# Kernel optimization log

Measured on AMD Instinct MI355X. Metric: run time of the kernel, lower is better.

The kernel has to match this reference:

```python
import jax, jax.numpy as jnp
import numpy as np

N_NODES = 100000
N_EDGES = 1250000
IN_FEATS = 64
OUT_FEATS = 64


def setup_inputs() -> dict:
    key = jax.random.key(0)
    k_h, k_src, k_dst, k_w, k_b = jax.random.split(key, 5)
    h = jax.random.normal(k_h, (N_NODES, IN_FEATS), dtype=jnp.float32)
    src = jax.random.randint(k_src, (N_EDGES,), 0, N_NODES, dtype=jnp.int64)
    dst = jax.random.randint(k_dst, (N_EDGES,), 0, N_NODES, dtype=jnp.int64)
    # torch nn.Linear: weight [out, in], bias [out], uniform(-stdv, stdv)
    stdv = 1.0 / np.sqrt(IN_FEATS)
    W = jax.random.uniform(k_w, (OUT_FEATS, IN_FEATS), dtype=jnp.float32, minval=-stdv, maxval=stdv)
    b = jax.random.uniform(k_b, (OUT_FEATS,), dtype=jnp.float32, minval=-stdv, maxval=stdv)
    return {"h": h, "src": src, "dst": dst, "W": W, "b": b}


def reference(h, src, dst, W, b):
    # update_all(copy_src, sum): ah[v] = sum over edges (u->v) of h[u]
    msgs = h[src]                                   # [E, in] irregular gather
    ah = jax.ops.segment_sum(msgs, dst, num_segments=N_NODES)  # [N, in] scatter-add
    out = ah @ W.T + b                              # linear
    return jax.nn.relu(out)
```

## Files before the change

kernel.cpp:

```cpp
#include <hip/hip_runtime.h>

#define N_NODES 100000
#define N_EDGES 1250000
#define FEATS 64

#define NPB   128
#define NBUCK ((N_NODES + NPB - 1) / NPB)
#define CAP   2304
#define TILE  4096
#define NTILES ((N_EDGES + TILE - 1) / TILE)

typedef unsigned short ushort8 __attribute__((ext_vector_type(8)));

__device__ __forceinline__ float bf2f(unsigned short u) {
    return __uint_as_float(((unsigned int)u) << 16);
}
__device__ __forceinline__ unsigned short f2bf(float f) {
    unsigned int x = __float_as_uint(f);
    unsigned int lsb = (x >> 16) & 1u;
    x += 0x7fffu + lsb;
    return (unsigned short)(x >> 16);
}


__global__ __launch_bounds__(256) void binA_pack_kernel(
        const float* __restrict__ h,
        unsigned short* __restrict__ hb,
        const int* __restrict__ src,
        const int* __restrict__ dst,
        int* __restrict__ cursor,
        int* __restrict__ pairs) {
    const int PTOT = N_NODES * FEATS;
    for (int i = (blockIdx.x * 256 + threadIdx.x) * 8; i < PTOT;
         i += gridDim.x * 256 * 8) {
        float4 a = *(const float4*)(h + i);
        float4 c = *(const float4*)(h + i + 4);
        ushort8 u;
        u[0] = f2bf(a.x); u[1] = f2bf(a.y); u[2] = f2bf(a.z); u[3] = f2bf(a.w);
        u[4] = f2bf(c.x); u[5] = f2bf(c.y); u[6] = f2bf(c.z); u[7] = f2bf(c.w);
        *(ushort8*)(hb + i) = u;
    }

    __shared__ int hist[NBUCK];
    __shared__ int base[NBUCK];
    const int t  = threadIdx.x;
    const int e0 = blockIdx.x * TILE + t * 16;
    const bool full = (blockIdx.x + 1) * TILE <= N_EDGES;

    for (int i = t; i < NBUCK; i += 256) hist[i] = 0;
    __syncthreads();

    int d[16], lr[16];
    if (full) {
#pragma unroll
        for (int q = 0; q < 4; ++q) {
            int4 v = *(const int4*)(dst + e0 + q * 4);
            d[q * 4 + 0] = v.x; d[q * 4 + 1] = v.y;
            d[q * 4 + 2] = v.z; d[q * 4 + 3] = v.w;
        }
#pragma unroll
        for (int j = 0; j < 16; ++j) lr[j] = atomicAdd(&hist[d[j] >> 7], 1);
    } else {
#pragma unroll
        for (int j = 0; j < 16; ++j) {
            if (e0 + j < N_EDGES) {
                d[j]  = dst[e0 + j];
                lr[j] = atomicAdd(&hist[d[j] >> 7], 1);
            }
        }
    }
    __syncthreads();

    for (int i = t; i < NBUCK; i += 256)
        base[i] = hist[i] ? atomicAdd(&cursor[i], hist[i]) : 0;
    __syncthreads();

    if (full) {
        int s[16];
#pragma unroll
        for (int q = 0; q < 4; ++q) {
            int4 v = *(const int4*)(src + e0 + q * 4);
            s[q * 4 + 0] = v.x; s[q * 4 + 1] = v.y;
            s[q * 4 + 2] = v.z; s[q * 4 + 3] = v.w;
        }
#pragma unroll
        for (int j = 0; j < 16; ++j) {
            int bk  = d[j] >> 7;
            int rel = base[bk] + lr[j];
            if (rel < CAP)
                pairs[(size_t)bk * CAP + rel] = (s[j] << 7) | (d[j] & (NPB - 1));
        }
    } else {
#pragma unroll
        for (int j = 0; j < 16; ++j) {
            if (e0 + j < N_EDGES) {
                int bk  = d[j] >> 7;
                int rel = base[bk] + lr[j];
                if (rel < CAP)
                    pairs[(size_t)bk * CAP + rel] =
                        (src[e0 + j] << 7) | (d[j] & (NPB - 1));
            }
        }
    }
}

__global__ __launch_bounds__(256) void agg_kernel(
        const unsigned short* __restrict__ hb,
        const int* __restrict__ pairs,
        const int* __restrict__ cursor,
        const float* __restrict__ W,
        const float* __restrict__ bias,
        float* __restrict__ out) {
    __shared__ int   ssrc[CAP];
    __shared__ int   lcnt[NPB];
    __shared__ int   loff[NPB + 1];
    __shared__ int   lcur[NPB];
    __shared__ float srow[4][8][FEATS];

    const int tid  = threadIdx.x;
    const int lane = tid & 63;
    const int wv   = tid >> 6;
    const int g    = lane >> 3;
    const int li   = lane & 7;
    const int fo   = li * 8;

    float wr[FEATS];
#pragma unroll
    for (int kk = 0; kk < 16; ++kk) {
        float4 w4 = *(const float4*)(W + (size_t)lane * FEATS + kk * 4);
        wr[kk * 4 + 0] = w4.x;
        wr[kk * 4 + 1] = w4.y;
        wr[kk * 4 + 2] = w4.z;
        wr[kk * 4 + 3] = w4.w;
    }
    const float bv = bias[lane];

    const int b = blockIdx.x;
    int size = cursor[b];
    if (size > CAP) size = CAP;
    const int* bp = pairs + (size_t)b * CAP;

    if (tid < NPB) lcnt[tid] = 0;
    __syncthreads();
    for (int i = tid; i < size; i += 256) atomicAdd(&lcnt[bp[i] & (NPB - 1)], 1);
    __syncthreads();
    if (tid < NPB) lcur[tid] = lcnt[tid];
    __syncthreads();
    for (int off = 1; off < NPB; off <<= 1) {
        int y = 0;
        if (tid < NPB && tid >= off) y = lcur[tid - off];
        __syncthreads();
        if (tid < NPB) lcur[tid] += y;
        __syncthreads();
    }
    if (tid < NPB) loff[tid + 1] = lcur[tid];
    if (tid == 0) loff[0] = 0;
    __syncthreads();
    if (tid < NPB) lcur[tid] = loff[tid];
    __syncthreads();
    for (int i = tid; i < size; i += 256) {
        int p = bp[i];
        int r = atomicAdd(&lcur[p & (NPB - 1)], 1);
        ssrc[r] = p >> 7;
    }
    __syncthreads();

#pragma unroll
    for (int pass = 0; pass < 4; ++pass) {
        const int ln  = pass * 32 + wv * 8 + g;
        const int beg = loff[ln];
        const int m   = loff[ln + 1] - beg;

        float acc0[8], acc1[8];
#pragma unroll
        for (int i = 0; i < 8; ++i) { acc0[i] = 0.f; acc1[i] = 0.f; }

        for (int base = 0; __any(base < m); base += 8) {
#pragma unroll
            for (int t = 0; t < 8; t += 2) {
                const int i0 = base + t, i1 = base + t + 1;
                int r0 = (i0 < m) ? ssrc[beg + i0] : 0;
                int r1 = (i1 < m) ? ssrc[beg + i1] : 0;
                if (i0 < m) {
                    ushort8 u = *(const ushort8*)(hb + (size_t)r0 * FEATS + fo);
#pragma unroll
                    for (int i = 0; i < 8; ++i) acc0[i] += bf2f(u[i]);
                }
                if (i1 < m) {
                    ushort8 u = *(const ushort8*)(hb + (size_t)r1 * FEATS + fo);
#pragma unroll
                    for (int i = 0; i < 8; ++i) acc1[i] += bf2f(u[i]);
                }
            }
        }
#pragma unroll
        for (int i = 0; i < 8; ++i) acc0[i] += acc1[i];

        *(float4*)&srow[wv][g][fo]     = make_float4(acc0[0], acc0[1], acc0[2], acc0[3]);
        *(float4*)&srow[wv][g][fo + 4] = make_float4(acc0[4], acc0[5], acc0[6], acc0[7]);

        const int n0 = b * NPB + pass * 32 + wv * 8;
#pragma unroll
        for (int gg = 0; gg < 8; ++gg) {
            const int nn = n0 + gg;
            if (nn >= N_NODES) break;
            const float4* ar = (const float4*)&srow[wv][gg][0];
            float o_acc = bv;
#pragma unroll
            for (int k4 = 0; k4 < 16; ++k4) {
                float4 r = ar[k4];
                o_acc = fmaf(r.x, wr[k4 * 4 + 0], o_acc);
                o_acc = fmaf(r.y, wr[k4 * 4 + 1], o_acc);
                o_acc = fmaf(r.z, wr[k4 * 4 + 2], o_acc);
                o_acc = fmaf(r.w, wr[k4 * 4 + 3], o_acc);
            }
            out[(size_t)nn * FEATS + lane] = fmaxf(o_acc, 0.0f);
        }
    }
}

extern "C" void kernel_launch(void* const* d_in, const int* in_sizes, int n_in,
                              void* d_out, int out_size, void* d_ws, size_t ws_size,
                              hipStream_t stream) {
    const float* h   = (const float*)d_in[0];
    const int*   src = (const int*)d_in[1];
    const int*   dst = (const int*)d_in[2];
    const float* W   = (const float*)d_in[3];
    const float* b   = (const float*)d_in[4];
    float* out = (float*)d_out;

    int* cursor = (int*)d_ws;
    int* pairs  = cursor + 1024;
    unsigned short* hb = (unsigned short*)(pairs + (size_t)NBUCK * CAP);

    hipMemsetAsync(cursor, 0, 1024 * sizeof(int), stream);
    binA_pack_kernel<<<NTILES, 256, 0, stream>>>(h, hb, src, dst, cursor, pairs);
    agg_kernel<<<NBUCK, 256, 0, stream>>>(hb, pairs, cursor, W, b, out);
}
```

Baseline: 159.6 us.

## Stage binned edges in LDS for coalesced writes; sort nodes by degree in aggregation

The binning kernel now builds a block-local prefix scan over buckets and stages each tile's packed pairs in shared memory in bucket order. The global writes to the pairs array therefore become contiguous runs per bucket instead of scattered stores. In the aggregation kernel, the nodes of each bucket are ranked by in-degree so the 8 nodes that share a wavefront have similar edge counts, which cuts divergence in the __any loop. The gather loop is also unrolled to 8 loads in flight with 4 accumulators. The cost is extra shared memory and synchronisation in the binning kernel, a multi-step scan over about 782 buckets, an O(128²) ranking step, and higher register pressure.

After: 194.4 us. 1.22x slower.

```diff
diff --git a/kernel.cpp b/kernel.cpp
--- a/kernel.cpp
+++ b/kernel.cpp
@@ -42,10 +42,16 @@
     }
 
     __shared__ int hist[NBUCK];
-    __shared__ int base[NBUCK];
-    const int t  = threadIdx.x;
-    const int e0 = blockIdx.x * TILE + t * 16;
-    const bool full = (blockIdx.x + 1) * TILE <= N_EDGES;
+    __shared__ int scn[NBUCK];
+    __shared__ int gbase[NBUCK];
+    __shared__ int stv[TILE];
+    __shared__ unsigned short stb[TILE];
+
+    const int t     = threadIdx.x;
+    const int tile0 = blockIdx.x * TILE;
+    const int tsize = (N_EDGES - tile0 < TILE) ? (N_EDGES - tile0) : TILE;
+    const bool full = (tsize == TILE);
+    const int e0 = tile0 + t * 16;
 
     for (int i = t; i < NBUCK; i += 256) hist[i] = 0;
     __syncthreads();
@@ -71,9 +77,20 @@
     }
     __syncthreads();
 
+    for (int i = t; i < NBUCK; i += 256) scn[i] = hist[i];
+    __syncthreads();
+    for (int off = 1; off < NBUCK; off <<= 1) {
+        int y[4];
+        int c = 0;
+        for (int i = t; i < NBUCK; i += 256) y[c++] = (i >= off) ? scn[i - off] : 0;
+        __syncthreads();
+        c = 0;
+        for (int i = t; i < NBUCK; i += 256) scn[i] += y[c++];
+        __syncthreads();
+    }
+
     for (int i = t; i < NBUCK; i += 256)
-        base[i] = hist[i] ? atomicAdd(&cursor[i], hist[i]) : 0;
-    __syncthreads();
+        gbase[i] = hist[i] ? atomicAdd(&cursor[i], hist[i]) : 0;
 
     if (full) {
         int s[16];
@@ -86,21 +103,28 @@
 #pragma unroll
         for (int j = 0; j < 16; ++j) {
             int bk  = d[j] >> 7;
-            int rel = base[bk] + lr[j];
-            if (rel < CAP)
-                pairs[(size_t)bk * CAP + rel] = (s[j] << 7) | (d[j] & (NPB - 1));
+            int pos = scn[bk] - hist[bk] + lr[j];
+            stv[pos] = (s[j] << 7) | (d[j] & (NPB - 1));
+            stb[pos] = (unsigned short)bk;
         }
     } else {
 #pragma unroll
         for (int j = 0; j < 16; ++j) {
             if (e0 + j < N_EDGES) {
                 int bk  = d[j] >> 7;
-                int rel = base[bk] + lr[j];
-                if (rel < CAP)
-                    pairs[(size_t)bk * CAP + rel] =
-                        (src[e0 + j] << 7) | (d[j] & (NPB - 1));
-            }
-        }
+                int pos = scn[bk] - hist[bk] + lr[j];
+                stv[pos] = (src[e0 + j] << 7) | (d[j] & (NPB - 1));
+                stb[pos] = (unsigned short)bk;
+            }
+        }
+    }
+    __syncthreads();
+
+    for (int i = t; i < tsize; i += 256) {
+        int bk  = stb[i];
+        int rel = gbase[bk] + (i - (scn[bk] - hist[bk]));
+        if (rel < CAP)
+            pairs[(size_t)bk * CAP + rel] = stv[i];
     }
 }
 
@@ -115,6 +139,7 @@
     __shared__ int   lcnt[NPB];
     __shared__ int   loff[NPB + 1];
     __shared__ int   lcur[NPB];
+    __shared__ int   slotNode[NPB];
     __shared__ float srow[4][8][FEATS];
 
     const int tid  = threadIdx.x;
@@ -163,58 +188,106 @@
         int r = atomicAdd(&lcur[p & (NPB - 1)], 1);
         ssrc[r] = p >> 7;
     }
+
+    if (tid < NPB) {
+        const int cnt = lcnt[tid];
+        int rank = 0;
+        for (int j = 0; j < NPB; ++j) {
+            int cj = lcnt[j];
+            rank += (cj > cnt) || (cj == cnt && j < tid);
+        }
+        slotNode[rank] = tid;
+    }
     __syncthreads();
 
 #pragma unroll
     for (int pass = 0; pass < 4; ++pass) {
-        const int ln  = pass * 32 + wv * 8 + g;
-        const int beg = loff[ln];
-        const int m   = loff[ln + 1] - beg;
-
-        float acc0[8], acc1[8];
-#pragma unroll
-        for (int i = 0; i < 8; ++i) { acc0[i] = 0.f; acc1[i] = 0.f; }
-
-        for (int base = 0; __any(base < m); base += 8) {
-#pragma unroll
-            for (int t = 0; t < 8; t += 2) {
-                const int i0 = base + t, i1 = base + t + 1;
-                int r0 = (i0 < m) ? ssrc[beg + i0] : 0;
-                int r1 = (i1 < m) ? ssrc[beg + i1] : 0;
-                if (i0 < m) {
-                    ushort8 u = *(const ushort8*)(hb + (size_t)r0 * FEATS + fo);
-#pragma unroll
-                    for (int i = 0; i < 8; ++i) acc0[i] += bf2f(u[i]);
-                }
-                if (i1 < m) {
-                    ushort8 u = *(const ushort8*)(hb + (size_t)r1 * FEATS + fo);
-#pragma unroll
-                    for (int i = 0; i < 8; ++i) acc1[i] += bf2f(u[i]);
-                }
-            }
-        }
-#pragma unroll
-        for (int i = 0; i < 8; ++i) acc0[i] += acc1[i];
+        const int slot = pass * 32 + wv * 8 + g;
+        const int ln   = slotNode[slot];
+        const int beg  = loff[ln];
+        const int m    = loff[ln + 1] - beg;
+
+        float acc0[8], acc1[8], acc2[8], acc3[8];
+#pragma unroll
+        for (int i = 0; i < 8; ++i) {
+            acc0[i] = 0.f; acc1[i] = 0.f; acc2[i] = 0.f; acc3[i] = 0.f;
+        }
+
+        for (int bb = 0; __any(bb < m); bb += 8) {
+            const int i0 = bb + 0, i1 = bb + 1, i2 = bb + 2, i3 = bb + 3;
+            const int i4 = bb + 4, i5 = bb + 5, i6 = bb + 6, i7 = bb + 7;
+            int r0 = (i0 < m) ? ssrc[beg + i0] : 0;
+            int r1 = (i1 < m) ? ssrc[beg + i1] : 0;
+            int r2 = (i2 < m) ? ssrc[beg + i2] : 0;
+            int r3 = (i3 < m) ? ssrc[beg + i3] : 0;
+            int r4 = (i4 < m) ? ssrc[beg + i4] : 0;
+            int r5 = (i5 < m) ? ssrc[beg + i5] : 0;
+            int r6 = (i6 < m) ? ssrc[beg + i6] : 0;
+            int r7 = (i7 < m) ? ssrc[beg + i7] : 0;
+            if (i0 < m) {
+                ushort8 u = *(const ushort8*)(hb + (size_t)r0 * FEATS + fo);
+#pragma unroll
+                for (int i = 0; i < 8; ++i) acc0[i] += bf2f(u[i]);
+            }
+            if (i1 < m) {
+                ushort8 u = *(const ushort8*)(hb + (size_t)r1 * FEATS + fo);
+#pragma unroll
+                for (int i = 0; i < 8; ++i) acc1[i] += bf2f(u[i]);
+            }
+            if (i2 < m) {
+                ushort8 u = *(const ushort8*)(hb + (size_t)r2 * FEATS + fo);
+#pragma unroll
+                for (int i = 0; i < 8; ++i) acc2[i] += bf2f(u[i]);
+            }
+            if (i3 < m) {
+                ushort8 u = *(const ushort8*)(hb + (size_t)r3 * FEATS + fo);
+#pragma unroll
+                for (int i = 0; i < 8; ++i) acc3[i] += bf2f(u[i]);
+            }
+            if (i4 < m) {
+                ushort8 u = *(const ushort8*)(hb + (size_t)r4 * FEATS + fo);
+#pragma unroll
+                for (int i = 0; i < 8; ++i) acc0[i] += bf2f(u[i]);
+            }
+            if (i5 < m) {
+                ushort8 u = *(const ushort8*)(hb + (size_t)r5 * FEATS + fo);
+#pragma unroll
+                for (int i = 0; i < 8; ++i) acc1[i] += bf2f(u[i]);
+            }
+            if (i6 < m) {
+                ushort8 u = *(const ushort8*)(hb + (size_t)r6 * FEATS + fo);
+#pragma unroll
+                for (int i = 0; i < 8; ++i) acc2[i] += bf2f(u[i]);
+            }
+            if (i7 < m) {
+                ushort8 u = *(const ushort8*)(hb + (size_t)r7 * FEATS + fo);
+#pragma unroll
+                for (int i = 0; i < 8; ++i) acc3[i] += bf2f(u[i]);
+            }
+        }
+#pragma unroll
+        for (int i = 0; i < 8; ++i) acc0[i] += acc1[i] + (acc2[i] + acc3[i]);
 
         *(float4*)&srow[wv][g][fo]     = make_float4(acc0[0], acc0[1], acc0[2], acc0[3]);
         *(float4*)&srow[wv][g][fo + 4] = make_float4(acc0[4], acc0[5], acc0[6], acc0[7]);
 
-        const int n0 = b * NPB + pass * 32 + wv * 8;
+        const int slotbase = pass * 32 + wv * 8;
 #pragma unroll
         for (int gg = 0; gg < 8; ++gg) {
-            const int nn = n0 + gg;
-            if (nn >= N_NODES) break;
-            const float4* ar = (const float4*)&srow[wv][gg][0];
-            float o_acc = bv;
-#pragma unroll
-            for (int k4 = 0; k4 < 16; ++k4) {
-                float4 r = ar[k4];
-                o_acc = fmaf(r.x, wr[k4 * 4 + 0], o_acc);
-                o_acc = fmaf(r.y, wr[k4 * 4 + 1], o_acc);
-                o_acc = fmaf(r.z, wr[k4 * 4 + 2], o_acc);
-                o_acc = fmaf(r.w, wr[k4 * 4 + 3], o_acc);
-            }
-            out[(size_t)nn * FEATS + lane] = fmaxf(o_acc, 0.0f);
+            const int nn = b * NPB + slotNode[slotbase + gg];
+            if (nn < N_NODES) {
+                const float4* ar = (const float4*)&srow[wv][gg][0];
+                float o_acc = bv;
+#pragma unroll
+                for (int k4 = 0; k4 < 16; ++k4) {
+                    float4 r = ar[k4];
+                    o_acc = fmaf(r.x, wr[k4 * 4 + 0], o_acc);
+                    o_acc = fmaf(r.y, wr[k4 * 4 + 1], o_acc);
+                    o_acc = fmaf(r.z, wr[k4 * 4 + 2], o_acc);
+                    o_acc = fmaf(r.w, wr[k4 * 4 + 3], o_acc);
+                }
+                out[(size_t)nn * FEATS + lane] = fmaxf(o_acc, 0.0f);
+            }
         }
     }
 }
```

## Apply linear transform before aggregation and gather transformed features

Applied to the files above, without the earlier changes.

Uses the linearity of the sum to compute h@W^T per node in a new pack kernel, storing the result as bf16, so the aggregation kernel only gathers, sums, adds bias and applies ReLU. This drops the per-node matvec and shared-memory staging from the aggregation kernel, which now writes coalesced float4 outputs. In exchange it adds a separate kernel launch and a per-node dense 64x64 matvec, and it splits the former combined pack/bin kernel in two. Rounding to bf16 now happens after the transform instead of before, which changes numerical error slightly.

New measurement: 193.3 us. 1.21x slower.

```diff
diff --git a/kernel.cpp b/kernel.cpp
--- a/kernel.cpp
+++ b/kernel.cpp
@@ -9,6 +9,7 @@
 #define CAP   2304
 #define TILE  4096
 #define NTILES ((N_EDGES + TILE - 1) / TILE)
+#define PK_BLOCKS ((N_NODES + 255) / 256)
 
 typedef unsigned short ushort8 __attribute__((ext_vector_type(8)));
 
@@ -23,24 +24,47 @@
 }
 
 
-__global__ __launch_bounds__(256) void binA_pack_kernel(
+__global__ __launch_bounds__(256) void pack_kernel(
         const float* __restrict__ h,
-        unsigned short* __restrict__ hb,
+        const float* __restrict__ W,
+        unsigned short* __restrict__ hwb) {
+    const int n = blockIdx.x * 256 + threadIdx.x;
+    if (n >= N_NODES) return;
+
+    float hr[FEATS];
+    const float4* hp = (const float4*)(h + (size_t)n * FEATS);
+#pragma unroll
+    for (int k4 = 0; k4 < 16; ++k4) {
+        float4 v = hp[k4];
+        hr[k4 * 4 + 0] = v.x; hr[k4 * 4 + 1] = v.y;
+        hr[k4 * 4 + 2] = v.z; hr[k4 * 4 + 3] = v.w;
+    }
+
+    for (int ob = 0; ob < 8; ++ob) {
+        ushort8 u;
+#pragma unroll
+        for (int oi = 0; oi < 8; ++oi) {
+            const float* wrow = W + (size_t)(ob * 8 + oi) * FEATS;
+            float acc = 0.f;
+#pragma unroll
+            for (int k4 = 0; k4 < 16; ++k4) {
+                float4 w = *(const float4*)(wrow + k4 * 4);
+                acc = fmaf(hr[k4 * 4 + 0], w.x, acc);
+                acc = fmaf(hr[k4 * 4 + 1], w.y, acc);
+                acc = fmaf(hr[k4 * 4 + 2], w.z, acc);
+                acc = fmaf(hr[k4 * 4 + 3], w.w, acc);
+            }
+            u[oi] = f2bf(acc);
+        }
+        *(ushort8*)(hwb + (size_t)n * FEATS + ob * 8) = u;
+    }
+}
+
+__global__ __launch_bounds__(256) void bin_kernel(
         const int* __restrict__ src,
         const int* __restrict__ dst,
         int* __restrict__ cursor,
         int* __restrict__ pairs) {
-    const int PTOT = N_NODES * FEATS;
-    for (int i = (blockIdx.x * 256 + threadIdx.x) * 8; i < PTOT;
-         i += gridDim.x * 256 * 8) {
-        float4 a = *(const float4*)(h + i);
-        float4 c = *(const float4*)(h + i + 4);
-        ushort8 u;
-        u[0] = f2bf(a.x); u[1] = f2bf(a.y); u[2] = f2bf(a.z); u[3] = f2bf(a.w);
-        u[4] = f2bf(c.x); u[5] = f2bf(c.y); u[6] = f2bf(c.z); u[7] = f2bf(c.w);
-        *(ushort8*)(hb + i) = u;
-    }
-
     __shared__ int hist[NBUCK];
     __shared__ int base[NBUCK];
     const int t  = threadIdx.x;
@@ -105,17 +129,15 @@
 }
 
 __global__ __launch_bounds__(256) void agg_kernel(
-        const unsigned short* __restrict__ hb,
+        const unsigned short* __restrict__ hwb,
         const int* __restrict__ pairs,
         const int* __restrict__ cursor,
-        const float* __restrict__ W,
         const float* __restrict__ bias,
         float* __restrict__ out) {
-    __shared__ int   ssrc[CAP];
-    __shared__ int   lcnt[NPB];
-    __shared__ int   loff[NPB + 1];
-    __shared__ int   lcur[NPB];
-    __shared__ float srow[4][8][FEATS];
+    __shared__ int ssrc[CAP];
+    __shared__ int lcnt[NPB];
+    __shared__ int loff[NPB + 1];
+    __shared__ int lcur[NPB];
 
     const int tid  = threadIdx.x;
     const int lane = tid & 63;
@@ -124,16 +146,8 @@
     const int li   = lane & 7;
     const int fo   = li * 8;
 
-    float wr[FEATS];
-#pragma unroll
-    for (int kk = 0; kk < 16; ++kk) {
-        float4 w4 = *(const float4*)(W + (size_t)lane * FEATS + kk * 4);
-        wr[kk * 4 + 0] = w4.x;
-        wr[kk * 4 + 1] = w4.y;
-        wr[kk * 4 + 2] = w4.z;
-        wr[kk * 4 + 3] = w4.w;
-    }
-    const float bv = bias[lane];
+    const float4 bv0 = *(const float4*)(bias + fo);
+    const float4 bv1 = *(const float4*)(bias + fo + 4);
 
     const int b = blockIdx.x;
     int size = cursor[b];
@@ -182,39 +196,32 @@
                 int r0 = (i0 < m) ? ssrc[beg + i0] : 0;
                 int r1 = (i1 < m) ? ssrc[beg + i1] : 0;
                 if (i0 < m) {
-                    ushort8 u = *(const ushort8*)(hb + (size_t)r0 * FEATS + fo);
+                    ushort8 u = *(const ushort8*)(hwb + (size_t)r0 * FEATS + fo);
 #pragma unroll
                     for (int i = 0; i < 8; ++i) acc0[i] += bf2f(u[i]);
                 }
                 if (i1 < m) {
-                    ushort8 u = *(const ushort8*)(hb + (size_t)r1 * FEATS + fo);
+                    ushort8 u = *(const ushort8*)(hwb + (size_t)r1 * FEATS + fo);
 #pragma unroll
                     for (int i = 0; i < 8; ++i) acc1[i] += bf2f(u[i]);
                 }
             }
         }
-#pragma unroll
-        for (int i = 0; i < 8; ++i) acc0[i] += acc1[i];
-
-        *(float4*)&srow[wv][g][fo]     = make_float4(acc0[0], acc0[1], acc0[2], acc0[3]);
-        *(float4*)&srow[wv][g][fo + 4] = make_float4(acc0[4], acc0[5], acc0[6], acc0[7]);
-
-        const int n0 = b * NPB + pass * 32 + wv * 8;
-#pragma unroll
-        for (int gg = 0; gg < 8; ++gg) {
-            const int nn = n0 + gg;
-            if (nn >= N_NODES) break;
-            const float4* ar = (const float4*)&srow[wv][gg][0];
-            float o_acc = bv;
-#pragma unroll
-            for (int k4 = 0; k4 < 16; ++k4) {
-                float4 r = ar[k4];
-                o_acc = fmaf(r.x, wr[k4 * 4 + 0], o_acc);
-                o_acc = fmaf(r.y, wr[k4 * 4 + 1], o_acc);
-                o_acc = fmaf(r.z, wr[k4 * 4 + 2], o_acc);
-                o_acc = fmaf(r.w, wr[k4 * 4 + 3], o_acc);
-            }
-            out[(size_t)nn * FEATS + lane] = fmaxf(o_acc, 0.0f);
+
+        const int nn = b * NPB + ln;
+        if (nn < N_NODES) {
+            float4 o0, o1;
+            o0.x = fmaxf(acc0[0] + acc1[0] + bv0.x, 0.f);
+            o0.y = fmaxf(acc0[1] + acc1[1] + bv0.y, 0.f);
+            o0.z = fmaxf(acc0[2] + acc1[2] + bv0.z, 0.f);
+            o0.w = fmaxf(acc0[3] + acc1[3] + bv0.w, 0.f);
+            o1.x = fmaxf(acc0[4] + acc1[4] + bv1.x, 0.f);
+            o1.y = fmaxf(acc0[5] + acc1[5] + bv1.y, 0.f);
+            o1.z = fmaxf(acc0[6] + acc1[6] + bv1.z, 0.f);
+            o1.w = fmaxf(acc0[7] + acc1[7] + bv1.w, 0.f);
+            float* op = out + (size_t)nn * FEATS + fo;
+            *(float4*)op       = o0;
+            *(float4*)(op + 4) = o1;
         }
     }
 }
@@ -231,9 +238,10 @@
 
     int* cursor = (int*)d_ws;
     int* pairs  = cursor + 1024;
-    unsigned short* hb = (unsigned short*)(pairs + (size_t)NBUCK * CAP);
+    unsigned short* hwb = (unsigned short*)(pairs + (size_t)NBUCK * CAP);
 
     hipMemsetAsync(cursor, 0, 1024 * sizeof(int), stream);
-    binA_pack_kernel<<<NTILES, 256, 0, stream>>>(h, hb, src, dst, cursor, pairs);
-    agg_kernel<<<NBUCK, 256, 0, stream>>>(hb, pairs, cursor, W, b, out);
-}
+    bin_kernel<<<NTILES, 256, 0, stream>>>(src, dst, cursor, pairs);
+    pack_kernel<<<PK_BLOCKS, 256, 0, stream>>>(h, W, hwb);
+    agg_kernel<<<NBUCK, 256, 0, stream>>>(hwb, pairs, cursor, b, out);
+}
```
